# Optimization experiments

Measured on AMD Instinct MI355X. Metric: run time of the kernel, lower is better.

## Reference

```python
import jax, jax.numpy as jnp
import numpy as np

B = 32768
N_EXPERTS = 5
K = 28  # kernel == image size, conv reduces to a full-image dot product


def setup_inputs() -> dict:
    key = jax.random.key(0)
    ks = jax.random.split(key, 6)
    x = jax.random.normal(ks[0], (B, 1, K, K), dtype=jnp.float32)
    category_indices = jax.random.randint(ks[1], (B,), 0, N_EXPERTS, dtype=jnp.int32)
    # expert conv weights: Conv2d(1,1,28) -> weight [1,1,28,28], bias [1]; stacked over 5 experts
    conv_w = jax.random.normal(ks[2], (N_EXPERTS, 1, K, K), dtype=jnp.float32) * 0.02
    conv_b = jax.random.normal(ks[3], (N_EXPERTS,), dtype=jnp.float32) * 0.02
    fc1_w = jax.random.normal(ks[4], (1, N_EXPERTS), dtype=jnp.float32) * 0.1
    fc1_b = jax.random.normal(ks[5], (1,), dtype=jnp.float32) * 0.1
    return {"x": x, "category_indices": category_indices, "conv_w": conv_w,
            "conv_b": conv_b, "fc1_w": fc1_w, "fc1_b": fc1_b}


def reference(x, category_indices, conv_w, conv_b, fc1_w, fc1_b):
    Bn = x.shape[0]
    # kernel size == image size with no padding -> each expert conv is a dot product over 784 pixels
    xf = x.reshape(Bn, -1)                      # [B, 784]
    wf = conv_w.reshape(N_EXPERTS, -1)          # [5, 784]
    w_sel = wf[category_indices]                # [B, 784] gather expert weight per sample
    b_sel = conv_b[category_indices]            # [B]
    s = jnp.einsum('bd,bd->b', xf, w_sel) + b_sel  # per-sample expert scalar output
    # scatter each scalar into the column of its expert; other columns stay zero
    stage1 = jnp.zeros((Bn, N_EXPERTS), dtype=x.dtype).at[jnp.arange(Bn), category_indices].set(s)
    out = jax.nn.relu(stage1 @ fc1_w.T + fc1_b)  # [B, 1]
    return out
```

## Files before the change

### kernel.cpp

```cpp
#include <hip/hip_runtime.h>

#define KK 784
#define NE 5

__global__ __launch_bounds__(256, 4) void moe_conv_fused_kernel(
    const float* __restrict__ x,
    const int*   __restrict__ cat,
    const float* __restrict__ conv_w,
    const float* __restrict__ conv_b,
    const float* __restrict__ fc1_w,
    const float* __restrict__ fc1_b,
    float*       __restrict__ out,
    int B)
{
    __shared__ float w_lds[NE * KK];
    __shared__ float cb_lds[NE];
    __shared__ float fw_lds[NE];

    {
        const float4* src = reinterpret_cast<const float4*>(conv_w);
        float4* dst = reinterpret_cast<float4*>(w_lds);
        for (int i = threadIdx.x; i < (NE * KK) / 4; i += blockDim.x)
            dst[i] = src[i];
        if (threadIdx.x < NE) {
            cb_lds[threadIdx.x] = conv_b[threadIdx.x];
            fw_lds[threadIdx.x] = fc1_w[threadIdx.x];
        }
    }
    __syncthreads();

    const float fb = fc1_b[0];
    const int lane   = threadIdx.x & 63;
    const int wave   = (blockIdx.x * blockDim.x + threadIdx.x) >> 6;
    const int nwaves = (gridDim.x * blockDim.x) >> 6;

    for (int s = wave; s < B; s += nwaves) {
        const int e = cat[s];
        const float4* xv = reinterpret_cast<const float4*>(x + (size_t)s * KK);
        const float4* wv = reinterpret_cast<const float4*>(w_lds + e * KK);

        float4 a0 = xv[lane];        float4 b0 = wv[lane];
        float4 a1 = xv[lane + 64];   float4 b1 = wv[lane + 64];
        float4 a2 = xv[lane + 128];  float4 b2 = wv[lane + 128];

        float acc;
        acc  = a0.x * b0.x + a0.y * b0.y + a0.z * b0.z + a0.w * b0.w;
        acc += a1.x * b1.x + a1.y * b1.y + a1.z * b1.z + a1.w * b1.w;
        acc += a2.x * b2.x + a2.y * b2.y + a2.z * b2.z + a2.w * b2.w;
        if (lane < 4) {
            float4 a3 = xv[192 + lane];
            float4 b3 = wv[192 + lane];
            acc += a3.x * b3.x + a3.y * b3.y + a3.z * b3.z + a3.w * b3.w;
        }

        #pragma unroll
        for (int off = 32; off > 0; off >>= 1)
            acc += __shfl_down(acc, off, 64);

        if (lane == 0) {
            const float sval = acc + cb_lds[e];
            const float o    = sval * fw_lds[e] + fb;
            out[s] = o > 0.0f ? o : 0.0f;
        }
    }
}

extern "C" void kernel_launch(void* const* d_in, const int* in_sizes, int n_in,
                              void* d_out, int out_size, void* d_ws, size_t ws_size,
                              hipStream_t stream) {
    const float* x      = (const float*)d_in[0];
    const int*   cat    = (const int*)d_in[1];
    const float* conv_w = (const float*)d_in[2];
    const float* conv_b = (const float*)d_in[3];
    const float* fc1_w  = (const float*)d_in[4];
    const float* fc1_b  = (const float*)d_in[5];
    float* out = (float*)d_out;

    const int B = in_sizes[1];

    const int block = 256;
    int grid = 2048;
    const int waves_needed = (B + 0) / 1;
    (void)waves_needed; (void)d_ws; (void)ws_size; (void)n_in; (void)out_size;
    if (grid * (block / 64) > B) grid = (B + (block / 64) - 1) / (block / 64);

    moe_conv_fused_kernel<<<grid, block, 0, stream>>>(
        x, cat, conv_w, conv_b, fc1_w, fc1_b, out, B);
}
```

Baseline: 22.81 us.

## Map four samples per wave with 16-lane groups and read weights from cache

Replaces the persistent grid-stride loop, where one wave handles one sample, with a one-shot grid in which each 16-lane group handles one sample. The LDS staging of all expert weights and the block barrier are removed, and weights are read directly from global memory through the cache. Each lane issues 12 or 13 float4 loads up front, giving more memory-level parallelism, and the shuffle reduction shrinks to 4 steps. The cost is higher register pressure and repeated global reads of the small weight table instead of LDS reads.

```diff
diff --git a/kernel.cpp b/kernel.cpp
--- a/kernel.cpp
+++ b/kernel.cpp
@@ -2,6 +2,10 @@
 
 #define KK 784
 #define NE 5
+
+__device__ __forceinline__ float dot4(float4 a, float4 b) {
+    return a.x * b.x + a.y * b.y + a.z * b.z + a.w * b.w;
+}
 
 __global__ __launch_bounds__(256, 4) void moe_conv_fused_kernel(
     const float* __restrict__ x,
@@ -13,55 +17,54 @@
     float*       __restrict__ out,
     int B)
 {
-    __shared__ float w_lds[NE * KK];
-    __shared__ float cb_lds[NE];
-    __shared__ float fw_lds[NE];
+    const int tid  = blockIdx.x * blockDim.x + threadIdx.x;
+    const int wid  = tid >> 6;
+    const int lane = threadIdx.x & 63;
+    const int grp  = lane >> 4;
+    const int sub  = lane & 15;
+    const int s    = wid * 4 + grp;
+    if (s >= B) return;
 
-    {
-        const float4* src = reinterpret_cast<const float4*>(conv_w);
-        float4* dst = reinterpret_cast<float4*>(w_lds);
-        for (int i = threadIdx.x; i < (NE * KK) / 4; i += blockDim.x)
-            dst[i] = src[i];
-        if (threadIdx.x < NE) {
-            cb_lds[threadIdx.x] = conv_b[threadIdx.x];
-            fw_lds[threadIdx.x] = fc1_w[threadIdx.x];
-        }
+    const int e = cat[s];
+    const float4* __restrict__ xv =
+        reinterpret_cast<const float4*>(x) + (size_t)s * (KK / 4);
+    const float4* __restrict__ wv =
+        reinterpret_cast<const float4*>(conv_w) + (size_t)e * (KK / 4);
+
+    float4 xa[12];
+    #pragma unroll
+    for (int i = 0; i < 12; ++i)
+        xa[i] = xv[sub + 16 * i];
+
+    const bool extra = (sub < 4);
+    float4 xt;
+    if (extra) xt = xv[192 + sub];
+
+    float a0 = 0.f, a1 = 0.f, a2 = 0.f, a3 = 0.f;
+    #pragma unroll
+    for (int i = 0; i < 12; i += 4) {
+        float4 w0 = wv[sub + 16 * (i + 0)];
+        float4 w1 = wv[sub + 16 * (i + 1)];
+        float4 w2 = wv[sub + 16 * (i + 2)];
+        float4 w3 = wv[sub + 16 * (i + 3)];
+        a0 += dot4(xa[i + 0], w0);
+        a1 += dot4(xa[i + 1], w1);
+        a2 += dot4(xa[i + 2], w2);
+        a3 += dot4(xa[i + 3], w3);
     }
-    __syncthreads();
+    if (extra) {
+        float4 wt = wv[192 + sub];
+        a0 += dot4(xt, wt);
+    }
+    float acc = (a0 + a1) + (a2 + a3);
 
-    const float fb = fc1_b[0];
-    const int lane   = threadIdx.x & 63;
-    const int wave   = (blockIdx.x * blockDim.x + threadIdx.x) >> 6;
-    const int nwaves = (gridDim.x * blockDim.x) >> 6;
+    #pragma unroll
+    for (int off = 8; off > 0; off >>= 1)
+        acc += __shfl_down(acc, off, 16);
 
-    for (int s = wave; s < B; s += nwaves) {
-        const int e = cat[s];
-        const float4* xv = reinterpret_cast<const float4*>(x + (size_t)s * KK);
-        const float4* wv = reinterpret_cast<const float4*>(w_lds + e * KK);
-
-        float4 a0 = xv[lane];        float4 b0 = wv[lane];
-        float4 a1 = xv[lane + 64];   float4 b1 = wv[lane + 64];
-        float4 a2 = xv[lane + 128];  float4 b2 = wv[lane + 128];
-
-        float acc;
-        acc  = a0.x * b0.x + a0.y * b0.y + a0.z * b0.z + a0.w * b0.w;
-        acc += a1.x * b1.x + a1.y * b1.y + a1.z * b1.z + a1.w * b1.w;
-        acc += a2.x * b2.x + a2.y * b2.y + a2.z * b2.z + a2.w * b2.w;
-        if (lane < 4) {
-            float4 a3 = xv[192 + lane];
-            float4 b3 = wv[192 + lane];
-            acc += a3.x * b3.x + a3.y * b3.y + a3.z * b3.z + a3.w * b3.w;
-        }
-
-        #pragma unroll
-        for (int off = 32; off > 0; off >>= 1)
-            acc += __shfl_down(acc, off, 64);
-
-        if (lane == 0) {
-            const float sval = acc + cb_lds[e];
-            const float o    = sval * fw_lds[e] + fb;
-            out[s] = o > 0.0f ? o : 0.0f;
-        }
+    if (sub == 0) {
+        float o = (acc + conv_b[e]) * fc1_w[e] + fc1_b[0];
+        out[s] = fmaxf(o, 0.0f);
     }
 }
 
@@ -77,12 +80,10 @@
     float* out = (float*)d_out;
 
     const int B = in_sizes[1];
+    (void)d_ws; (void)ws_size; (void)n_in; (void)out_size;
 
     const int block = 256;
-    int grid = 2048;
-    const int waves_needed = (B + 0) / 1;
-    (void)waves_needed; (void)d_ws; (void)ws_size; (void)n_in; (void)out_size;
-    if (grid * (block / 64) > B) grid = (B + (block / 64) - 1) / (block / 64);
+    const int grid  = (B + 15) / 16;
 
     moe_conv_fused_kernel<<<grid, block, 0, stream>>>(
         x, cat, conv_w, conv_b, fc1_w, fc1_b, out, B);
```

After: 20.93 us. -8.3%, faster.
